# Performance work log

Hardware: AMD Instinct MI355X
Metric: run time of the kernel (lower is better)

Reference implementation:

```python
import jax, jax.numpy as jnp
import numpy as np

IN_DIM = 128
OUT_DIM = 256
N_ETYPES = 4
N_STEPS = 8
B = 128
N_NODES = 256
E = 393216
CONCAT = IN_DIM + OUT_DIM


def _conv1d(x, w, b):
    # x: [B, C, L], w: [O, I, K] -> valid conv, stride 1
    y = jax.lax.conv_general_dilated(x, w, (1,), 'VALID', dimension_numbers=('NCH', 'OIH', 'NCH'))
    return y + b[None, :, None]


def _maxpool1d(x, k, s):
    return jax.lax.reduce_window(x, -jnp.inf, jax.lax.max, (1, 1, k), (1, 1, s), 'VALID')


def setup_inputs():
    key = jax.random.key(0)
    ks = jax.random.split(key, 16)
    Nn = B * N_NODES
    sc = 0.05
    f32 = jnp.float32
    return {
        'features': jax.random.normal(ks[0], (Nn, IN_DIM), f32),
        'src': jax.random.randint(ks[1], (E,), 0, Nn),
        'dst': jax.random.randint(ks[2], (E,), 0, Nn),
        'etype': jax.random.randint(ks[3], (E,), 0, N_ETYPES),
        'W_msg': jax.random.normal(ks[4], (N_ETYPES, OUT_DIM, OUT_DIM), f32) * sc,
        'b_msg': jnp.zeros((N_ETYPES, OUT_DIM), f32),
        'gru_Wi': jax.random.normal(ks[5], (OUT_DIM, 3 * OUT_DIM), f32) * sc,
        'gru_Wh': jax.random.normal(ks[6], (OUT_DIM, 3 * OUT_DIM), f32) * sc,
        'gru_bi': jnp.zeros((3 * OUT_DIM,), f32),
        'gru_bh': jnp.zeros((3 * OUT_DIM,), f32),
        'conv1_w': jax.random.normal(ks[7], (OUT_DIM, OUT_DIM, 3), f32) * sc,
        'conv1_b': jnp.zeros((OUT_DIM,), f32),
        'conv2_w': jax.random.normal(ks[8], (OUT_DIM, OUT_DIM, 1), f32) * sc,
        'conv2_b': jnp.zeros((OUT_DIM,), f32),
        'convc1_w': jax.random.normal(ks[9], (CONCAT, CONCAT, 3), f32) * sc,
        'convc1_b': jnp.zeros((CONCAT,), f32),
        'convc2_w': jax.random.normal(ks[10], (CONCAT, CONCAT, 1), f32) * sc,
        'convc2_b': jnp.zeros((CONCAT,), f32),
        'wy': jax.random.normal(ks[11], (OUT_DIM, 1), f32) * sc,
        'by': jnp.zeros((1,), f32),
        'wz': jax.random.normal(ks[12], (CONCAT, 1), f32) * sc,
        'bz': jnp.zeros((1,), f32),
        'num_graphs': B,
    }


def reference(features, src, dst, etype, W_msg, b_msg, gru_Wi, gru_Wh, gru_bi, gru_bh,
              conv1_w, conv1_b, conv2_w, conv2_b, convc1_w, convc1_b, convc2_w, convc2_b,
              wy, by, wz, bz, num_graphs):
    Nn = features.shape[0]
    # DGL GatedGraphConv: pad input feats up to out_feats
    h = jnp.pad(features, ((0, 0), (0, OUT_DIM - IN_DIM)))
    for _ in range(N_STEPS):
        # per-etype linear transform of all nodes: [Nn, T, O]
        H_all = jnp.einsum('nd,tdo->nto', h, W_msg) + b_msg[None]
        msg = H_all[src, etype]                              # [E, O]
        a = jax.ops.segment_sum(msg, dst, num_segments=Nn)   # [Nn, O]
        gi = a @ gru_Wi + gru_bi
        gh = h @ gru_Wh + gru_bh
        ir, iz, ig = jnp.split(gi, 3, axis=-1)
        hr, hz, hg = jnp.split(gh, 3, axis=-1)
        r = jax.nn.sigmoid(ir + hr)
        z = jax.nn.sigmoid(iz + hz)
        g = jnp.tanh(ig + r * hg)
        h = (1.0 - z) * g + z * h
    x_i = features.reshape(num_graphs, -1, IN_DIM)
    h_i = h.reshape(num_graphs, -1, OUT_DIM)
    c_i = jnp.concatenate([h_i, x_i], axis=-1)
    Y1 = _maxpool1d(jax.nn.relu(_conv1d(h_i.transpose(0, 2, 1), conv1_w, conv1_b)), 3, 2)
    Y2 = _maxpool1d(jax.nn.relu(_conv1d(Y1, conv2_w, conv2_b)), 2, 2).transpose(0, 2, 1)
    Z1 = _maxpool1d(jax.nn.relu(_conv1d(c_i.transpose(0, 2, 1), convc1_w, convc1_b)), 3, 2)
    Z2 = _maxpool1d(jax.nn.relu(_conv1d(Z1, convc2_w, convc2_b)), 2, 2).transpose(0, 2, 1)
    before_avg = (Y2 @ wy + by) * (Z2 @ wz + bz)   # [B, L, 1]
    avg = before_avg.mean(axis=1)                    # [B, 1]
    return jax.nn.sigmoid(avg).squeeze(-1)           # [B]
```

## Files before the change

### kernel.cpp

```cpp
#include <hip/hip_runtime.h>

#define DEV static __device__ __forceinline__

typedef float f32x4 __attribute__((ext_vector_type(4)));
typedef __bf16 bf16x8 __attribute__((ext_vector_type(8)));
typedef unsigned int u32x4 __attribute__((ext_vector_type(4)));
typedef unsigned int u32x2 __attribute__((ext_vector_type(2)));

#define NNODE 32768
#define NEDGE 393216
#define EPAD (NEDGE + 8 * NNODE)

DEV unsigned short f2bf(float f) {
    unsigned int u = __builtin_bit_cast(unsigned int, f);
    u += 0x7FFFu + ((u >> 16) & 1u);
    return (unsigned short)(u >> 16);
}
DEV float bf2f(unsigned int b) {
    unsigned int u = b << 16;
    return __builtin_bit_cast(float, u);
}
DEV unsigned int pk2(float a, float b) {
    return (unsigned int)f2bf(a) | ((unsigned int)f2bf(b) << 16);
}
DEV float sigf(float x) { return 1.f / (1.f + __expf(-x)); }

DEV void gld16(const void* g, void* l) {
    __builtin_amdgcn_global_load_lds(
        (const __attribute__((address_space(1))) void*)(g),
        (__attribute__((address_space(3))) void*)(l),
        16, 0, 0);
}


__global__ __launch_bounds__(256) void init_k(
    const float* __restrict__ feat,
    unsigned short* __restrict__ hb0, unsigned short* __restrict__ hb1,
    unsigned short* __restrict__ fb)
{
    int idx = blockIdx.x * 256 + threadIdx.x;
    int r = idx >> 8, c = idx & 255;
    float f = 0.f;
    if (r < NNODE && c < 128) f = feat[(size_t)r * 128 + c];
    unsigned short v = f2bf(f);
    hb0[(size_t)r * 256 + c] = v;
    hb1[(size_t)r * 256 + c] = v;
    if (c < 128) fb[(size_t)r * 128 + c] = v;
}

__global__ __launch_bounds__(256) void prep_wmsg_k(
    const float* __restrict__ Wm, unsigned short* __restrict__ WT)
{
    int idx = blockIdx.x * 256 + threadIdx.x;
    int j = idx >> 8, d = idx & 255;
    int t = j >> 8, o = j & 255;
    WT[idx] = f2bf(Wm[t * 65536 + d * 256 + o]);
}

__global__ __launch_bounds__(256) void prep_gru_k(
    const float* __restrict__ Wi, const float* __restrict__ Wh,
    unsigned short* __restrict__ B2T)
{
    int idx = blockIdx.x * 256 + threadIdx.x;
    int j = idx >> 9, k = idx & 511;
    int band = j >> 6, g = (j >> 4) & 3, ch = (band << 4) + (j & 15);
    float v = 0.f;
    if (g == 0) v = (k < 256) ? Wi[k * 768 + ch] : Wh[(k - 256) * 768 + ch];
    else if (g == 1) v = (k < 256) ? Wi[k * 768 + 256 + ch] : Wh[(k - 256) * 768 + 256 + ch];
    else if (g == 2) { if (k < 256) v = Wi[k * 768 + 512 + ch]; }
    else { if (k >= 256) v = Wh[(k - 256) * 768 + 512 + ch]; }
    B2T[idx] = f2bf(v);
}

__global__ __launch_bounds__(256) void prep_bias2_k(
    const float* __restrict__ bi, const float* __restrict__ bh,
    float* __restrict__ b2)
{
    int j = blockIdx.x * 256 + threadIdx.x;
    int band = j >> 6, g = (j >> 4) & 3, ch = (band << 4) + (j & 15);
    float v;
    if (g == 0) v = bi[ch] + bh[ch];
    else if (g == 1) v = bi[256 + ch] + bh[256 + ch];
    else if (g == 2) v = bi[512 + ch];
    else v = bh[512 + ch];
    b2[j] = v;
}

__global__ __launch_bounds__(256) void prep_conv_k(
    const float* __restrict__ c1w, const float* __restrict__ c2w,
    const float* __restrict__ cc1w, const float* __restrict__ cc2w,
    unsigned short* __restrict__ BTY, unsigned short* __restrict__ BT2,
    unsigned short* __restrict__ BTZ, unsigned short* __restrict__ BTc2)
{
    int idx = blockIdx.x * 256 + threadIdx.x;
    if (idx < 196608) {
        int o = idx / 768, kk = idx - o * 768, k = kk >> 8, c = kk & 255;
        BTY[idx] = f2bf(c1w[o * 768 + c * 3 + k]);
    } else if (idx < 262144) {
        int r = idx - 196608, o = r >> 8, c = r & 255;
        BT2[r] = f2bf(c2w[o * 256 + c]);
    } else if (idx < 704512) {
        int jx = idx - 262144, o = jx / 1152, kk = jx - o * 1152;
        float v;
        if (kk < 768) { int k = kk >> 8, c = kk & 255; v = cc1w[o * 1152 + c * 3 + k]; }
        else { int r = kk - 768, kf = r >> 7, cf = r & 127; v = cc1w[o * 1152 + (256 + cf) * 3 + kf]; }
        BTZ[jx] = f2bf(v);
    } else {
        int r = idx - 704512, o = r / 384, c = r - o * 384;
        BTc2[r] = f2bf(cc2w[o * 384 + c]);
    }
}


__global__ __launch_bounds__(256) void pad_k(int* __restrict__ edat)
{
    edat[blockIdx.x * 256 + threadIdx.x] = NNODE;
}

__global__ __launch_bounds__(256) void count_k(
    const int* __restrict__ dst, int* __restrict__ cnt)
{
    int e = blockIdx.x * 256 + threadIdx.x;
    atomicAdd(&cnt[dst[e]], 1);
}

__global__ __launch_bounds__(1024) void scan1_k(
    const int* __restrict__ cnt, int* __restrict__ rp, int* __restrict__ bsum)
{
    __shared__ int buf[1024];
    int b = blockIdx.x, tid = threadIdx.x;
    int n = (b << 10) + tid;
    int v = (cnt[n] + 7) & ~7;
    buf[tid] = v;
    __syncthreads();
    for (int off = 1; off < 1024; off <<= 1) {
        int x = (tid >= off) ? buf[tid - off] : 0;
        __syncthreads();
        buf[tid] += x;
        __syncthreads();
    }
    rp[n] = buf[tid] - v;
    if (tid == 1023) bsum[b] = buf[1023];
}

__global__ __launch_bounds__(64) void scan2_k(
    const int* __restrict__ bsum, int* __restrict__ boff, int* __restrict__ rp)
{
    int lane = threadIdx.x;
    int v = (lane < 32) ? bsum[lane] : 0;
    int s = v;
    #pragma unroll
    for (int off = 1; off < 32; off <<= 1) {
        int x = __shfl_up(s, off, 64);
        if (lane >= off) s += x;
    }
    if (lane < 32) boff[lane] = s - v;
    if (lane == 31) rp[NNODE] = s;
}

__global__ __launch_bounds__(1024) void scan3_k(
    int* __restrict__ rp, const int* __restrict__ boff)
{
    int b = blockIdx.x, tid = threadIdx.x;
    rp[(b << 10) + tid] += boff[b];
}

__global__ __launch_bounds__(256) void fill_k(
    const int* __restrict__ src, const int* __restrict__ dst,
    const int* __restrict__ et, const int* __restrict__ rp,
    int* __restrict__ pos, int* __restrict__ edat)
{
    int e = blockIdx.x * 256 + threadIdx.x;
    int d = dst[e];
    int p = atomicAdd(&pos[d], 1);
    edat[rp[d] + p] = src[e] | (et[e] << 20);
}


__global__ __launch_bounds__(256) void agg2_k(
    const int* __restrict__ rp, const int* __restrict__ edat,
    const unsigned short* __restrict__ Hmsg, unsigned short* __restrict__ Aonly)
{
    int wave = threadIdx.x >> 6, lane = threadIdx.x & 63;
    int n = (blockIdx.x << 2) + wave;
    int e0 = rp[n], e1 = rp[n + 1];
    float a0 = 0.f, a1 = 0.f, a2 = 0.f, a3 = 0.f;
    const unsigned short* hc = Hmsg + (lane << 2);
    for (int e = e0; e < e1; e += 8) {
        u32x2 v[8];
        #pragma unroll
        for (int q = 0; q < 8; q++) {
            int d = edat[e + q];
            v[q] = *(const u32x2*)(hc + ((size_t)(d & 0xFFFFF) << 10) + ((d >> 20) << 8));
        }
        #pragma unroll
        for (int q = 0; q < 8; q++) {
            a0 += bf2f(v[q].x & 0xFFFFu); a1 += bf2f(v[q].x >> 16);
            a2 += bf2f(v[q].y & 0xFFFFu); a3 += bf2f(v[q].y >> 16);
        }
    }
    u32x2 p; p.x = pk2(a0, a1); p.y = pk2(a2, a3);
    *(u32x2*)(Aonly + (size_t)n * 256 + (lane << 2)) = p;
}

#define STAGE_COORDS                                            \
    int srow[4], scb[4], soff[4];                               \
    _Pragma("unroll")                                           \
    for (int p = 0; p < 4; p++) {                               \
        int c = wave + p * 4;                                   \
        int half = c >> 3, cc = c & 7;                          \
        srow[p] = cc * 16 + (lane >> 2);                        \
        scb[p] = (((lane & 3) ^ ((lane >> 3) & 3)) + half * 4) * 8; \
        soff[p] = half * 4096 + cc * 512;                       \
    }

#define MFMA64(AS, BS)                                                        \
    _Pragma("unroll")                                                         \
    for (int h = 0; h < 2; h++) {                                             \
        bf16x8 af[4], bfr[4];                                                 \
        _Pragma("unroll")                                                     \
        for (int i = 0; i < 4; i++)                                           \
            af[i] = *(const bf16x8*)(&(AS)[h * 4096 + (qm + i * 16 + fm) * 32 + fksw * 8]); \
        _Pragma("unroll")                                                     \
        for (int i = 0; i < 4; i++)                                           \
            bfr[i] = *(const bf16x8*)(&(BS)[h * 4096 + (qn + i * 16 + fm) * 32 + fksw * 8]); \
        _Pragma("unroll")                                                     \
        for (int i = 0; i < 4; i++)                                           \
            _Pragma("unroll")                                                 \
            for (int j = 0; j < 4; j++)                                       \
                acc[i][j] = __builtin_amdgcn_mfma_f32_16x16x32_bf16(bfr[j], af[i], acc[i][j], 0, 0, 0); \
    }

#define MFMA64G(AS, BS, SK)                                                   \
    _Pragma("unroll")                                                         \
    for (int h = 0; h < 2; h++) {                                             \
        bf16x8 af[4], bfr[4];                                                 \
        _Pragma("unroll")                                                     \
        for (int i = 0; i < 4; i++)                                           \
            af[i] = *(const bf16x8*)(&(AS)[h * 4096 + (qm + i * 16 + fm) * 32 + fksw * 8]); \
        _Pragma("unroll")                                                     \
        for (int j = 0; j < 4; j++) {                                         \
            if (j == (SK)) continue;                                          \
            bfr[j] = *(const bf16x8*)(&(BS)[h * 4096 + (qn + j * 16 + fm) * 32 + fksw * 8]); \
        }                                                                     \
        _Pragma("unroll")                                                     \
        for (int i = 0; i < 4; i++)                                           \
            _Pragma("unroll")                                                 \
            for (int j = 0; j < 4; j++) {                                     \
                if (j == (SK)) continue;                                      \
                acc[i][j] = __builtin_amdgcn_mfma_f32_16x16x32_bf16(bfr[j], af[i], acc[i][j], 0, 0, 0); \
            }                                                                 \
    }

__global__ __launch_bounds__(256) void gemm_hmsg(
    const unsigned short* __restrict__ A,
    const unsigned short* __restrict__ Bt,
    unsigned short* __restrict__ Cb,
    const float* __restrict__ bias)
{
    __shared__ __align__(16) unsigned short As0[128 * 64];
    __shared__ __align__(16) unsigned short As1[128 * 64];
    __shared__ __align__(16) unsigned short Bs0[128 * 64];
    __shared__ __align__(16) unsigned short Bs1[128 * 64];
    const int tid = threadIdx.x;
    int id = blockIdx.x;
    { int per = gridDim.x >> 3; id = (id & 7) * per + (id >> 3); }
    const int bm = id >> 3, bn = id & 7;
    const int wave = tid >> 6, lane = tid & 63;
    const unsigned short* Ag = A + (size_t)(bm * 128) * 256;
    const unsigned short* Bg = Bt + (size_t)(bn * 128) * 256;
    const int qm = (wave & 1) << 6, qn = (wave >> 1) << 6;
    const int fm = lane & 15, fkv = lane >> 4;
    const int fksw = fkv ^ ((fm >> 1) & 3);
    STAGE_COORDS

    auto stageA = [&](int kb, unsigned short* dst) {
        #pragma unroll
        for (int p = 0; p < 4; p++)
            gld16(Ag + (size_t)srow[p] * 256 + kb + scb[p], dst + soff[p]);
    };
    auto stageB = [&](int kb, unsigned short* dst) {
        #pragma unroll
        for (int p = 0; p < 4; p++)
            gld16(Bg + (size_t)srow[p] * 256 + kb + scb[p], dst + soff[p]);
    };

    f32x4 acc[4][4] = {};

    stageA(0, As0); stageB(0, Bs0);
    __syncthreads();
    unsigned short *Ac = As0, *An = As1, *Bc = Bs0, *Bn = Bs1;
    #pragma unroll
    for (int kb = 0; kb < 256; kb += 64) {
        if (kb < 192) { stageA(kb + 64, An); stageB(kb + 64, Bn); }
        MFMA64(Ac, Bc)
        __syncthreads();
        { auto t = Ac; Ac = An; An = t; }
        { auto t = Bc; Bc = Bn; Bn = t; }
    }

    const int m0 = bm * 128 + qm + fm;
    const int n0 = bn * 128 + qn + (fkv << 2);
    #pragma unroll
    for (int i = 0; i < 4; i++) {
        int row = m0 + i * 16;
        #pragma unroll
        for (int j = 0; j < 4; j++) {
            int col = n0 + j * 16;
            float4 bv = *(const float4*)(bias + col);
            u32x2 p;
            p.x = pk2(acc[i][j][0] + bv.x, acc[i][j][1] + bv.y);
            p.y = pk2(acc[i][j][2] + bv.z, acc[i][j][3] + bv.w);
            *(u32x2*)(Cb + (size_t)row * 1024 + col) = p;
        }
    }
}

__global__ __launch_bounds__(256) void gemm_bt(
    const unsigned short* __restrict__ A, int lda,
    const unsigned short* __restrict__ Bt,
    unsigned short* __restrict__ Cb, int ldcb,
    const float* __restrict__ bias,
    int N, int K, int swz, int relu)
{
    __shared__ __align__(16) unsigned short As0[128 * 64];
    __shared__ __align__(16) unsigned short As1[128 * 64];
    __shared__ __align__(16) unsigned short Bs0[128 * 64];
    __shared__ __align__(16) unsigned short Bs1[128 * 64];
    const int tid = threadIdx.x;
    int id = blockIdx.x;
    if (swz) { int per = gridDim.x >> 3; id = (id & 7) * per + (id >> 3); }
    const int nb = N >> 7;
    const int bm = id / nb, bn = id - bm * nb;
    const int wave = tid >> 6, lane = tid & 63;
    const unsigned short* Ag = A + (size_t)(bm * 128) * lda;
    const unsigned short* Bg = Bt + (size_t)(bn * 128) * K;
    const int qm = (wave & 1) << 6, qn = (wave >> 1) << 6;
    const int fm = lane & 15, fkv = lane >> 4;
    const int fksw = fkv ^ ((fm >> 1) & 3);
    STAGE_COORDS

    auto stageA = [&](int kb, unsigned short* dst) {
        #pragma unroll
        for (int p = 0; p < 4; p++)
            gld16(Ag + (size_t)srow[p] * lda + kb + scb[p], dst + soff[p]);
    };
    auto stageB = [&](int kb, unsigned short* dst) {
        #pragma unroll
        for (int p = 0; p < 4; p++)
            gld16(Bg + (size_t)srow[p] * K + kb + scb[p], dst + soff[p]);
    };

    f32x4 acc[4][4] = {};

    stageA(0, As0); stageB(0, Bs0);
    __syncthreads();
    unsigned short *Ac = As0, *An = As1, *Bc = Bs0, *Bn = Bs1;
    for (int kb = 0; kb < K; kb += 64) {
        if (kb + 64 < K) { stageA(kb + 64, An); stageB(kb + 64, Bn); }
        MFMA64(Ac, Bc)
        __syncthreads();
        { auto t = Ac; Ac = An; An = t; }
        { auto t = Bc; Bc = Bn; Bn = t; }
    }

    const int m0 = bm * 128 + qm + fm;
    const int n0 = bn * 128 + qn + (fkv << 2);
    #pragma unroll
    for (int i = 0; i < 4; i++) {
        int row = m0 + i * 16;
        #pragma unroll
        for (int j = 0; j < 4; j++) {
            int col = n0 + j * 16;
            float v0 = acc[i][j][0], v1 = acc[i][j][1],
                  v2 = acc[i][j][2], v3 = acc[i][j][3];
            if (bias) {
                float4 bv = *(const float4*)(bias + col);
                v0 += bv.x; v1 += bv.y; v2 += bv.z; v3 += bv.w;
            }
            if (relu) {
                v0 = fmaxf(v0, 0.f); v1 = fmaxf(v1, 0.f);
                v2 = fmaxf(v2, 0.f); v3 = fmaxf(v3, 0.f);
            }
            u32x2 p; p.x = pk2(v0, v1); p.y = pk2(v2, v3);
            *(u32x2*)(Cb + (size_t)row * ldcb + col) = p;
        }
    }
}

__global__ __launch_bounds__(256) void gemm_conv(
    const unsigned short* __restrict__ Ah,
    const unsigned short* __restrict__ Af,
    const unsigned short* __restrict__ Bt,
    unsigned short* __restrict__ Cb, int ldcb,
    const float* __restrict__ bias,
    int N, int K)
{
    __shared__ __align__(16) unsigned short As0[128 * 64];
    __shared__ __align__(16) unsigned short As1[128 * 64];
    __shared__ __align__(16) unsigned short Bs0[128 * 64];
    __shared__ __align__(16) unsigned short Bs1[128 * 64];
    const int tid = threadIdx.x;
    int id = blockIdx.x;
    { int per = gridDim.x >> 3; id = (id & 7) * per + (id >> 3); }
    const int nb = N >> 7;
    const int bm = id / nb, bn = id - bm * nb;
    const int wave = tid >> 6, lane = tid & 63;
    const unsigned short* Bg = Bt + (size_t)(bn * 128) * K;
    const int qm = (wave & 1) << 6, qn = (wave >> 1) << 6;
    const int fm = lane & 15, fkv = lane >> 4;
    const int fksw = fkv ^ ((fm >> 1) & 3);
    STAGE_COORDS

    auto stageA = [&](int kb, unsigned short* dst) {
        const unsigned short* base; int ldA, col, shift;
        if (kb < 768) { base = Ah; ldA = 256; shift = kb >> 8; col = kb & 255; }
        else { int r = kb - 768; base = Af; ldA = 128; shift = r >> 7; col = r & 127; }
        const unsigned short* Ag = base + (size_t)(bm * 128 + shift) * ldA + col;
        #pragma unroll
        for (int p = 0; p < 4; p++)
            gld16(Ag + (size_t)srow[p] * ldA + scb[p], dst + soff[p]);
    };
    auto stageB = [&](int kb, unsigned short* dst) {
        #pragma unroll
        for (int p = 0; p < 4; p++)
            gld16(Bg + (size_t)srow[p] * K + kb + scb[p], dst + soff[p]);
    };

    f32x4 acc[4][4] = {};

    stageA(0, As0); stageB(0, Bs0);
    __syncthreads();
    unsigned short *Ac = As0, *An = As1, *Bc = Bs0, *Bn = Bs1;
    for (int kb = 0; kb < K; kb += 64) {
        if (kb + 64 < K) { stageA(kb + 64, An); stageB(kb + 64, Bn); }
        MFMA64(Ac, Bc)
        __syncthreads();
        { auto t = Ac; Ac = An; An = t; }
        { auto t = Bc; Bc = Bn; Bn = t; }
    }

    const int m0 = bm * 128 + qm + fm;
    const int n0 = bn * 128 + qn + (fkv << 2);
    #pragma unroll
    for (int i = 0; i < 4; i++) {
        int row = m0 + i * 16;
        #pragma unroll
        for (int j = 0; j < 4; j++) {
            int col = n0 + j * 16;
            float4 bv = *(const float4*)(bias + col);
            float v0 = fmaxf(acc[i][j][0] + bv.x, 0.f);
            float v1 = fmaxf(acc[i][j][1] + bv.y, 0.f);
            float v2 = fmaxf(acc[i][j][2] + bv.z, 0.f);
            float v3 = fmaxf(acc[i][j][3] + bv.w, 0.f);
            u32x2 p; p.x = pk2(v0, v1); p.y = pk2(v2, v3);
            *(u32x2*)(Cb + (size_t)row * ldcb + col) = p;
        }
    }
}

__global__ __launch_bounds__(256) void gemm_gru(
    const unsigned short* __restrict__ Aonly,
    const unsigned short* __restrict__ hbc,
    const unsigned short* __restrict__ Bt,
    const float* __restrict__ b2p,
    unsigned short* __restrict__ hbn)
{
    __shared__ __align__(16) unsigned short As0[128 * 64];
    __shared__ __align__(16) unsigned short As1[128 * 64];
    __shared__ __align__(16) unsigned short Bs0[128 * 64];
    __shared__ __align__(16) unsigned short Bs1[128 * 64];
    const int tid = threadIdx.x;
    int id = blockIdx.x;
    { int per = gridDim.x >> 3; id = (id & 7) * per + (id >> 3); }
    const int bm = id >> 3;
    const int bn = id & 7;
    const int wave = tid >> 6, lane = tid & 63;
    const unsigned short* Bg = Bt + (size_t)(bn * 128) * 512;
    const int qm = (wave & 1) << 6, qn = (wave >> 1) << 6;
    const int fm = lane & 15, fkv = lane >> 4;
    const int fksw = fkv ^ ((fm >> 1) & 3);
    STAGE_COORDS

    auto stageA = [&](int kb, unsigned short* dst) {
        const unsigned short* base = (kb < 256) ? Aonly : hbc;
        const unsigned short* Ag = base + (size_t)(bm * 128) * 256 + (kb & 255);
        #pragma unroll
        for (int p = 0; p < 4; p++)
            gld16(Ag + (size_t)srow[p] * 256 + scb[p], dst + soff[p]);
    };
    auto stageB = [&](int kb, unsigned short* dst) {
        #pragma unroll
        for (int p = 0; p < 4; p++)
            gld16(Bg + (size_t)srow[p] * 512 + kb + scb[p], dst + soff[p]);
    };

    f32x4 acc[4][4] = {};

    stageA(0, As0); stageB(0, Bs0);
    __syncthreads();
    unsigned short *Ac = As0, *An = As1, *Bc = Bs0, *Bn = Bs1;
    #pragma unroll
    for (int kb = 0; kb < 512; kb += 64) {
        if (kb < 448) { stageA(kb + 64, An); stageB(kb + 64, Bn); }
        if (kb < 256) { MFMA64G(Ac, Bc, 3) }
        else          { MFMA64G(Ac, Bc, 2) }
        __syncthreads();
        { auto t = Ac; Ac = An; An = t; }
        { auto t = Bc; Bc = Bn; Bn = t; }
    }

    const int band = (bn << 1) + (qn >> 6);
    const int chb = (band << 4) + (fkv << 2);
    const float4 brv = *(const float4*)(b2p + (band << 6) + 0  + (fkv << 2));
    const float4 bzv = *(const float4*)(b2p + (band << 6) + 16 + (fkv << 2));
    const float4 bgv = *(const float4*)(b2p + (band << 6) + 32 + (fkv << 2));
    const float4 bhv = *(const float4*)(b2p + (band << 6) + 48 + (fkv << 2));
    const float br_[4] = {brv.x, brv.y, brv.z, brv.w};
    const float bz_[4] = {bzv.x, bzv.y, bzv.z, bzv.w};
    const float bg_[4] = {bgv.x, bgv.y, bgv.z, bgv.w};
    const float bh_[4] = {bhv.x, bhv.y, bhv.z, bhv.w};
    const int m0 = bm * 128 + qm + fm;
    #pragma unroll
    for (int i = 0; i < 4; i++) {
        int row = m0 + i * 16;
        u32x2 hv = *(const u32x2*)(hbc + (size_t)row * 256 + chb);
        float hp[4] = {bf2f(hv.x & 0xFFFFu), bf2f(hv.x >> 16),
                       bf2f(hv.y & 0xFFFFu), bf2f(hv.y >> 16)};
        float hn[4];
        #pragma unroll
        for (int r = 0; r < 4; r++) {
            float rg = sigf(acc[i][0][r] + br_[r]);
            float zz = sigf(acc[i][1][r] + bz_[r]);
            float pre = acc[i][2][r] + bg_[r] + rg * (acc[i][3][r] + bh_[r]);
            pre = fminf(fmaxf(pre, -15.f), 15.f);
            float t = __expf(2.f * pre);
            float gq = (t - 1.f) / (t + 1.f);
            hn[r] = (1.f - zz) * gq + zz * hp[r];
        }
        u32x2 p; p.x = pk2(hn[0], hn[1]); p.y = pk2(hn[2], hn[3]);
        *(u32x2*)(hbn + (size_t)row * 256 + chb) = p;
    }
}

__global__ __launch_bounds__(256) void pool_k(
    const unsigned short* __restrict__ in, int ldin, int Lb_in, int L_out,
    int win, int C,
    unsigned short* __restrict__ ob, int ldo)
{
    int idx = blockIdx.x * 256 + threadIdx.x;
    int c = idx % C;
    int row = idx / C;
    int b = row / L_out, lp = row - b * L_out;
    const unsigned short* p = in + (size_t)(b * Lb_in + 2 * lp) * ldin + c;
    float m = bf2f(p[0]);
    for (int d = 1; d < win; d++) m = fmaxf(m, bf2f(p[(size_t)d * ldin]));
    ob[(size_t)row * ldo + c] = f2bf(m);
}

__global__ __launch_bounds__(64) void final_k(
    const unsigned short* __restrict__ CY, const unsigned short* __restrict__ CZ,
    const float* __restrict__ wy, const float* __restrict__ by,
    const float* __restrict__ wz, const float* __restrict__ bz,
    float* __restrict__ out)
{
    int b = blockIdx.x, lane = threadIdx.x;
    float val = 0.f;
    if (lane < 63) {
        const unsigned short* y0 = CY + (size_t)(b * 126 + 2 * lane) * 256;
        const unsigned short* y1 = y0 + 256;
        float y = 0.f;
        for (int o = 0; o < 256; o++)
            y += fmaxf(bf2f(y0[o]), bf2f(y1[o])) * wy[o];
        y += by[0];
        const unsigned short* z0 = CZ + (size_t)(b * 126 + 2 * lane) * 384;
        const unsigned short* z1 = z0 + 384;
        float z = 0.f;
        for (int o = 0; o < 384; o++)
            z += fmaxf(bf2f(z0[o]), bf2f(z1[o])) * wz[o];
        z += bz[0];
        val = y * z;
    }
    for (int off = 32; off > 0; off >>= 1) val += __shfl_down(val, off, 64);
    if (lane == 0) out[b] = sigf(val * (1.f / 63.f));
}


extern "C" void kernel_launch(void* const* d_in, const int* in_sizes, int n_in,
                              void* d_out, int out_size, void* d_ws, size_t ws_size,
                              hipStream_t stream)
{
    const float* feat = (const float*)d_in[0];
    const int* src = (const int*)d_in[1];
    const int* dst = (const int*)d_in[2];
    const int* et  = (const int*)d_in[3];
    const float* Wm  = (const float*)d_in[4];
    const float* bm  = (const float*)d_in[5];
    const float* Wi  = (const float*)d_in[6];
    const float* Wh  = (const float*)d_in[7];
    const float* bi  = (const float*)d_in[8];
    const float* bh  = (const float*)d_in[9];
    const float* c1w = (const float*)d_in[10];
    const float* c1b = (const float*)d_in[11];
    const float* c2w = (const float*)d_in[12];
    const float* c2b = (const float*)d_in[13];
    const float* cc1w = (const float*)d_in[14];
    const float* cc1b = (const float*)d_in[15];
    const float* cc2w = (const float*)d_in[16];
    const float* cc2b = (const float*)d_in[17];
    const float* wy = (const float*)d_in[18];
    const float* by = (const float*)d_in[19];
    const float* wz = (const float*)d_in[20];
    const float* bz = (const float*)d_in[21];
    float* out = (float*)d_out;

    char* w = (char*)d_ws;
    size_t off = 0;
    auto alloc = [&](size_t bytes) -> char* {
        char* p = w + off; off += (bytes + 255) & ~(size_t)255; return p;
    };
    unsigned short* hb0 = (unsigned short*)alloc((size_t)(NNODE + 8) * 256 * 2);
    unsigned short* hb1 = (unsigned short*)alloc((size_t)(NNODE + 8) * 256 * 2);
    unsigned short* fb  = (unsigned short*)alloc((size_t)(NNODE + 8) * 128 * 2);
    unsigned short* Aonly = (unsigned short*)alloc((size_t)NNODE * 256 * 2);
    char* R = alloc((size_t)(NNODE + 1) * 1024 * 2);
    unsigned short* Hmsg = (unsigned short*)R;
    unsigned short* CbY  = (unsigned short*)R;
    unsigned short* CbZ  = (unsigned short*)(R + (size_t)NNODE * 256 * 2);
    unsigned short* P    = (unsigned short*)alloc((size_t)16128 * 384 * 2);
    unsigned short* Cb2Y = (unsigned short*)alloc((size_t)16128 * 256 * 2);
    unsigned short* Cb2Z = (unsigned short*)alloc((size_t)16128 * 384 * 2);
    unsigned short* WT   = (unsigned short*)alloc(1024 * 256 * 2);
    unsigned short* B2T  = (unsigned short*)alloc(1024 * 512 * 2);
    float* b2            = (float*)alloc(1024 * 4);
    unsigned short* BTY  = (unsigned short*)alloc(256 * 768 * 2);
    unsigned short* BT2  = (unsigned short*)alloc(256 * 256 * 2);
    unsigned short* BTZ  = (unsigned short*)alloc(384 * 1152 * 2);
    unsigned short* BTc2 = (unsigned short*)alloc(384 * 384 * 2);
    int* rp     = (int*)alloc((NNODE + 1) * 4);
    int* pos    = (int*)alloc(NNODE * 4);
    int* cnt    = (int*)alloc(NNODE * 4);
    int* bsum   = (int*)alloc(32 * 4);
    int* boff   = (int*)alloc(32 * 4);
    int* edat   = (int*)alloc((size_t)EPAD * 4);

    hipLaunchKernelGGL(init_k, dim3(NNODE + 8), dim3(256), 0, stream, feat, hb0, hb1, fb);
    hipLaunchKernelGGL(prep_wmsg_k, dim3(1024), dim3(256), 0, stream, Wm, WT);
    hipLaunchKernelGGL(prep_gru_k, dim3(2048), dim3(256), 0, stream, Wi, Wh, B2T);
    hipLaunchKernelGGL(prep_bias2_k, dim3(4), dim3(256), 0, stream, bi, bh, b2);
    hipLaunchKernelGGL(prep_conv_k, dim3(3328), dim3(256), 0, stream,
                       c1w, c2w, cc1w, cc2w, BTY, BT2, BTZ, BTc2);
    hipMemsetAsync(pos, 0, NNODE * 4, stream);
    hipMemsetAsync(cnt, 0, NNODE * 4, stream);
    hipMemsetAsync(Hmsg + (size_t)NNODE * 1024, 0, 1024 * 2, stream);
    hipLaunchKernelGGL(pad_k, dim3(EPAD / 256), dim3(256), 0, stream, edat);
    hipLaunchKernelGGL(count_k, dim3(NEDGE / 256), dim3(256), 0, stream, dst, cnt);
    hipLaunchKernelGGL(scan1_k, dim3(32), dim3(1024), 0, stream, cnt, rp, bsum);
    hipLaunchKernelGGL(scan2_k, dim3(1), dim3(64), 0, stream, bsum, boff, rp);
    hipLaunchKernelGGL(scan3_k, dim3(32), dim3(1024), 0, stream, rp, boff);
    hipLaunchKernelGGL(fill_k, dim3(NEDGE / 256), dim3(256), 0, stream, src, dst, et, rp, pos, edat);

    unsigned short* hbuf[2] = {hb0, hb1};
    for (int step = 0; step < 8; step++) {
        unsigned short* cur = hbuf[step & 1];
        unsigned short* nxt = hbuf[(step + 1) & 1];
        hipLaunchKernelGGL(gemm_hmsg, dim3(2048), dim3(256), 0, stream,
            cur, WT, Hmsg, bm);
        hipLaunchKernelGGL(agg2_k, dim3(NNODE / 4), dim3(256), 0, stream, rp, edat, Hmsg, Aonly);
        hipLaunchKernelGGL(gemm_gru, dim3(2048), dim3(256), 0, stream,
            Aonly, cur, B2T, b2, nxt);
    }

    hipLaunchKernelGGL(gemm_conv, dim3(512), dim3(256), 0, stream,
        hb0, (const unsigned short*)nullptr, BTY, CbY, 256, c1b, 256, 768);
    hipLaunchKernelGGL(pool_k, dim3(16128), dim3(256), 0, stream,
        CbY, 256, 256, 126, 3, 256, P, 256);
    hipLaunchKernelGGL(gemm_bt, dim3(252), dim3(256), 0, stream,
        P, 256, BT2, Cb2Y, 256, c2b, 256, 256, 0, 1);

    hipLaunchKernelGGL(gemm_conv, dim3(768), dim3(256), 0, stream,
        hb0, fb, BTZ, CbZ, 384, cc1b, 384, 1152);
    hipLaunchKernelGGL(pool_k, dim3(24192), dim3(256), 0, stream,
        CbZ, 384, 256, 126, 3, 384, P, 384);
    hipLaunchKernelGGL(gemm_bt, dim3(378), dim3(256), 0, stream,
        P, 384, BTc2, Cb2Z, 384, cc2b, 384, 384, 0, 1);

    hipLaunchKernelGGL(final_k, dim3(128), dim3(64), 0, stream,
        Cb2Y, Cb2Z, wy, by, wz, bz, out);
}
```

Measured before the change: 1.192 ms.

## Fuse prep kernels, widen aggregation loads, skip zero-padded K in first step

Merges the four weight-prep kernels into one launch and folds the edge-padding fill into the count kernel. The block-offset scan pass is removed; consumers add the block offset themselves. Aggregation now uses 16-byte loads with two edges per lane-half, padding segments to 16 and combining halves with a shuffle. Step 0 GEMMs skip the zero upper half of the padded input K-range, and the final reduction is parallelised across 256 threads. Padding to 16 adds dummy edge reads for low-degree nodes.

```diff
diff --git a/kernel.cpp b/kernel.cpp
--- a/kernel.cpp
+++ b/kernel.cpp
@@ -9,7 +9,7 @@
 
 #define NNODE 32768
 #define NEDGE 393216
-#define EPAD (NEDGE + 8 * NNODE)
+#define EPAD (NEDGE + 16 * NNODE)
 
 DEV unsigned short f2bf(float f) {
     unsigned int u = __builtin_bit_cast(unsigned int, f);
@@ -48,80 +48,70 @@
     if (c < 128) fb[(size_t)r * 128 + c] = v;
 }
 
-__global__ __launch_bounds__(256) void prep_wmsg_k(
-    const float* __restrict__ Wm, unsigned short* __restrict__ WT)
-{
-    int idx = blockIdx.x * 256 + threadIdx.x;
-    int j = idx >> 8, d = idx & 255;
-    int t = j >> 8, o = j & 255;
-    WT[idx] = f2bf(Wm[t * 65536 + d * 256 + o]);
-}
-
-__global__ __launch_bounds__(256) void prep_gru_k(
+__global__ __launch_bounds__(256) void prep_all_k(
+    const float* __restrict__ Wm,
     const float* __restrict__ Wi, const float* __restrict__ Wh,
-    unsigned short* __restrict__ B2T)
-{
-    int idx = blockIdx.x * 256 + threadIdx.x;
-    int j = idx >> 9, k = idx & 511;
-    int band = j >> 6, g = (j >> 4) & 3, ch = (band << 4) + (j & 15);
-    float v = 0.f;
-    if (g == 0) v = (k < 256) ? Wi[k * 768 + ch] : Wh[(k - 256) * 768 + ch];
-    else if (g == 1) v = (k < 256) ? Wi[k * 768 + 256 + ch] : Wh[(k - 256) * 768 + 256 + ch];
-    else if (g == 2) { if (k < 256) v = Wi[k * 768 + 512 + ch]; }
-    else { if (k >= 256) v = Wh[(k - 256) * 768 + 512 + ch]; }
-    B2T[idx] = f2bf(v);
-}
-
-__global__ __launch_bounds__(256) void prep_bias2_k(
     const float* __restrict__ bi, const float* __restrict__ bh,
-    float* __restrict__ b2)
-{
-    int j = blockIdx.x * 256 + threadIdx.x;
-    int band = j >> 6, g = (j >> 4) & 3, ch = (band << 4) + (j & 15);
-    float v;
-    if (g == 0) v = bi[ch] + bh[ch];
-    else if (g == 1) v = bi[256 + ch] + bh[256 + ch];
-    else if (g == 2) v = bi[512 + ch];
-    else v = bh[512 + ch];
-    b2[j] = v;
-}
-
-__global__ __launch_bounds__(256) void prep_conv_k(
     const float* __restrict__ c1w, const float* __restrict__ c2w,
     const float* __restrict__ cc1w, const float* __restrict__ cc2w,
+    unsigned short* __restrict__ WT, unsigned short* __restrict__ B2T,
+    float* __restrict__ b2,
     unsigned short* __restrict__ BTY, unsigned short* __restrict__ BT2,
     unsigned short* __restrict__ BTZ, unsigned short* __restrict__ BTc2)
 {
-    int idx = blockIdx.x * 256 + threadIdx.x;
-    if (idx < 196608) {
-        int o = idx / 768, kk = idx - o * 768, k = kk >> 8, c = kk & 255;
-        BTY[idx] = f2bf(c1w[o * 768 + c * 3 + k]);
-    } else if (idx < 262144) {
-        int r = idx - 196608, o = r >> 8, c = r & 255;
-        BT2[r] = f2bf(c2w[o * 256 + c]);
-    } else if (idx < 704512) {
-        int jx = idx - 262144, o = jx / 1152, kk = jx - o * 1152;
+    int gid = blockIdx.x * 256 + threadIdx.x;
+    if (gid < 262144) {
+        int idx = gid;
+        int j = idx >> 8, d = idx & 255;
+        int t = j >> 8, o = j & 255;
+        WT[idx] = f2bf(Wm[t * 65536 + d * 256 + o]);
+    } else if (gid < 786432) {
+        int idx = gid - 262144;
+        int j = idx >> 9, k = idx & 511;
+        int band = j >> 6, g = (j >> 4) & 3, ch = (band << 4) + (j & 15);
+        float v = 0.f;
+        if (g == 0) v = (k < 256) ? Wi[k * 768 + ch] : Wh[(k - 256) * 768 + ch];
+        else if (g == 1) v = (k < 256) ? Wi[k * 768 + 256 + ch] : Wh[(k - 256) * 768 + 256 + ch];
+        else if (g == 2) { if (k < 256) v = Wi[k * 768 + 512 + ch]; }
+        else { if (k >= 256) v = Wh[(k - 256) * 768 + 512 + ch]; }
+        B2T[idx] = f2bf(v);
+    } else if (gid < 787456) {
+        int j = gid - 786432;
+        int band = j >> 6, g = (j >> 4) & 3, ch = (band << 4) + (j & 15);
         float v;
-        if (kk < 768) { int k = kk >> 8, c = kk & 255; v = cc1w[o * 1152 + c * 3 + k]; }
-        else { int r = kk - 768, kf = r >> 7, cf = r & 127; v = cc1w[o * 1152 + (256 + cf) * 3 + kf]; }
-        BTZ[jx] = f2bf(v);
+        if (g == 0) v = bi[ch] + bh[ch];
+        else if (g == 1) v = bi[256 + ch] + bh[256 + ch];
+        else if (g == 2) v = bi[512 + ch];
+        else v = bh[512 + ch];
+        b2[j] = v;
     } else {
-        int r = idx - 704512, o = r / 384, c = r - o * 384;
-        BTc2[r] = f2bf(cc2w[o * 384 + c]);
-    }
-}
-
-
-__global__ __launch_bounds__(256) void pad_k(int* __restrict__ edat)
-{
-    edat[blockIdx.x * 256 + threadIdx.x] = NNODE;
-}
-
-__global__ __launch_bounds__(256) void count_k(
-    const int* __restrict__ dst, int* __restrict__ cnt)
+        int idx = gid - 787456;
+        if (idx < 196608) {
+            int o = idx / 768, kk = idx - o * 768, k = kk >> 8, c = kk & 255;
+            BTY[idx] = f2bf(c1w[o * 768 + c * 3 + k]);
+        } else if (idx < 262144) {
+            int r = idx - 196608, o = r >> 8, c = r & 255;
+            BT2[r] = f2bf(c2w[o * 256 + c]);
+        } else if (idx < 704512) {
+            int jx = idx - 262144, o = jx / 1152, kk = jx - o * 1152;
+            float v;
+            if (kk < 768) { int k = kk >> 8, c = kk & 255; v = cc1w[o * 1152 + c * 3 + k]; }
+            else { int r = kk - 768, kf = r >> 7, cf = r & 127; v = cc1w[o * 1152 + (256 + cf) * 3 + kf]; }
+            BTZ[jx] = f2bf(v);
+        } else {
+            int r = idx - 704512, o = r / 384, c = r - o * 384;
+            BTc2[r] = f2bf(cc2w[o * 384 + c]);
+        }
+    }
+}
+
+
+__global__ __launch_bounds__(256) void pc_k(
+    const int* __restrict__ dst, int* __restrict__ cnt, int* __restrict__ edat)
 {
     int e = blockIdx.x * 256 + threadIdx.x;
-    atomicAdd(&cnt[dst[e]], 1);
+    edat[e] = NNODE;
+    if (e < NEDGE) atomicAdd(&cnt[dst[e]], 1);
 }
 
 __global__ __launch_bounds__(1024) void scan1_k(
@@ -130,7 +120,7 @@
     __shared__ int buf[1024];
     int b = blockIdx.x, tid = threadIdx.x;
     int n = (b << 10) + tid;
-    int v = (cnt[n] + 7) & ~7;
+    int v = (cnt[n] + 15) & ~15;
     buf[tid] = v;
     __syncthreads();
     for (int off = 1; off < 1024; off <<= 1) {
@@ -155,52 +145,61 @@
         if (lane >= off) s += x;
     }
     if (lane < 32) boff[lane] = s - v;
+    if (lane == 32) boff[32] = 0;
     if (lane == 31) rp[NNODE] = s;
-}
-
-__global__ __launch_bounds__(1024) void scan3_k(
-    int* __restrict__ rp, const int* __restrict__ boff)
-{
-    int b = blockIdx.x, tid = threadIdx.x;
-    rp[(b << 10) + tid] += boff[b];
 }
 
 __global__ __launch_bounds__(256) void fill_k(
     const int* __restrict__ src, const int* __restrict__ dst,
     const int* __restrict__ et, const int* __restrict__ rp,
+    const int* __restrict__ boff,
     int* __restrict__ pos, int* __restrict__ edat)
 {
     int e = blockIdx.x * 256 + threadIdx.x;
     int d = dst[e];
     int p = atomicAdd(&pos[d], 1);
-    edat[rp[d] + p] = src[e] | (et[e] << 20);
+    edat[rp[d] + boff[d >> 10] + p] = src[e] | (et[e] << 20);
 }
 
 
 __global__ __launch_bounds__(256) void agg2_k(
-    const int* __restrict__ rp, const int* __restrict__ edat,
+    const int* __restrict__ rp, const int* __restrict__ boff,
+    const int* __restrict__ edat,
     const unsigned short* __restrict__ Hmsg, unsigned short* __restrict__ Aonly)
 {
     int wave = threadIdx.x >> 6, lane = threadIdx.x & 63;
     int n = (blockIdx.x << 2) + wave;
-    int e0 = rp[n], e1 = rp[n + 1];
+    int e0 = rp[n] + boff[n >> 10];
+    int e1 = rp[n + 1] + boff[(n + 1) >> 10];
+    int half = lane >> 5, lc = lane & 31;
     float a0 = 0.f, a1 = 0.f, a2 = 0.f, a3 = 0.f;
-    const unsigned short* hc = Hmsg + (lane << 2);
-    for (int e = e0; e < e1; e += 8) {
-        u32x2 v[8];
+    float a4 = 0.f, a5 = 0.f, a6 = 0.f, a7 = 0.f;
+    const unsigned short* hc = Hmsg + (lc << 3);
+    for (int e = e0; e < e1; e += 16) {
+        u32x4 v[8];
         #pragma unroll
         for (int q = 0; q < 8; q++) {
-            int d = edat[e + q];
-            v[q] = *(const u32x2*)(hc + ((size_t)(d & 0xFFFFF) << 10) + ((d >> 20) << 8));
+            int d = edat[e + (q << 1) + half];
+            v[q] = *(const u32x4*)(hc + ((size_t)(d & 0xFFFFF) << 10) + ((d >> 20) << 8));
         }
         #pragma unroll
         for (int q = 0; q < 8; q++) {
             a0 += bf2f(v[q].x & 0xFFFFu); a1 += bf2f(v[q].x >> 16);
             a2 += bf2f(v[q].y & 0xFFFFu); a3 += bf2f(v[q].y >> 16);
+            a4 += bf2f(v[q].z & 0xFFFFu); a5 += bf2f(v[q].z >> 16);
+            a6 += bf2f(v[q].w & 0xFFFFu); a7 += bf2f(v[q].w >> 16);
         }
     }
-    u32x2 p; p.x = pk2(a0, a1); p.y = pk2(a2, a3);
-    *(u32x2*)(Aonly + (size_t)n * 256 + (lane << 2)) = p;
+    a0 += __shfl_xor(a0, 32, 64); a1 += __shfl_xor(a1, 32, 64);
+    a2 += __shfl_xor(a2, 32, 64); a3 += __shfl_xor(a3, 32, 64);
+    a4 += __shfl_xor(a4, 32, 64); a5 += __shfl_xor(a5, 32, 64);
+    a6 += __shfl_xor(a6, 32, 64); a7 += __shfl_xor(a7, 32, 64);
+    if (half == 0) {
+        u32x4 p;
+        p.x = pk2(a0, a1); p.y = pk2(a2, a3);
+        p.z = pk2(a4, a5); p.w = pk2(a6, a7);
+        *(u32x4*)(Aonly + (size_t)n * 256 + (lc << 3)) = p;
+    }
 }
 
 #define STAGE_COORDS                                            \
@@ -252,6 +251,7 @@
             }                                                                 \
     }
 
+template<int NT>
 __global__ __launch_bounds__(256) void gemm_hmsg(
     const unsigned short* __restrict__ A,
     const unsigned short* __restrict__ Bt,
@@ -291,8 +291,8 @@
     __syncthreads();
     unsigned short *Ac = As0, *An = As1, *Bc = Bs0, *Bn = Bs1;
     #pragma unroll
-    for (int kb = 0; kb < 256; kb += 64) {
-        if (kb < 192) { stageA(kb + 64, An); stageB(kb + 64, Bn); }
+    for (int kb = 0; kb < NT * 64; kb += 64) {
+        if (kb + 64 < NT * 64) { stageA(kb + 64, An); stageB(kb + 64, Bn); }
         MFMA64(Ac, Bc)
         __syncthreads();
         { auto t = Ac; Ac = An; An = t; }
@@ -459,6 +459,7 @@
     }
 }
 
+template<int NT>
 __global__ __launch_bounds__(256) void gemm_gru(
     const unsigned short* __restrict__ Aonly,
     const unsigned short* __restrict__ hbc,
@@ -501,8 +502,8 @@
     __syncthreads();
     unsigned short *Ac = As0, *An = As1, *Bc = Bs0, *Bn = Bs1;
     #pragma unroll
-    for (int kb = 0; kb < 512; kb += 64) {
-        if (kb < 448) { stageA(kb + 64, An); stageB(kb + 64, Bn); }
+    for (int kb = 0; kb < NT * 64; kb += 64) {
+        if (kb + 64 < NT * 64) { stageA(kb + 64, An); stageB(kb + 64, Bn); }
         if (kb < 256) { MFMA64G(Ac, Bc, 3) }
         else          { MFMA64G(Ac, Bc, 2) }
         __syncthreads();
@@ -558,31 +559,48 @@
     ob[(size_t)row * ldo + c] = f2bf(m);
 }
 
-__global__ __launch_bounds__(64) void final_k(
+__global__ __launch_bounds__(256) void final_k(
     const unsigned short* __restrict__ CY, const unsigned short* __restrict__ CZ,
     const float* __restrict__ wy, const float* __restrict__ by,
     const float* __restrict__ wz, const float* __restrict__ bz,
     float* __restrict__ out)
 {
-    int b = blockIdx.x, lane = threadIdx.x;
-    float val = 0.f;
-    if (lane < 63) {
-        const unsigned short* y0 = CY + (size_t)(b * 126 + 2 * lane) * 256;
+    __shared__ float ws[4];
+    int b = blockIdx.x, tid = threadIdx.x;
+    int wave = tid >> 6, lane = tid & 63;
+    float wyv[4], wzv[6];
+    #pragma unroll
+    for (int j = 0; j < 4; j++) wyv[j] = wy[lane * 4 + j];
+    #pragma unroll
+    for (int j = 0; j < 6; j++) wzv[j] = wz[lane * 6 + j];
+    const float byv = by[0], bzv = bz[0];
+    float acc = 0.f;
+    for (int l = wave; l < 63; l += 4) {
+        const unsigned short* y0 = CY + (size_t)(b * 126 + 2 * l) * 256 + lane * 4;
         const unsigned short* y1 = y0 + 256;
-        float y = 0.f;
-        for (int o = 0; o < 256; o++)
-            y += fmaxf(bf2f(y0[o]), bf2f(y1[o])) * wy[o];
-        y += by[0];
-        const unsigned short* z0 = CZ + (size_t)(b * 126 + 2 * lane) * 384;
+        u32x2 u0 = *(const u32x2*)y0, u1 = *(const u32x2*)y1;
+        float py =
+            fmaxf(bf2f(u0.x & 0xFFFFu), bf2f(u1.x & 0xFFFFu)) * wyv[0] +
+            fmaxf(bf2f(u0.x >> 16),     bf2f(u1.x >> 16))     * wyv[1] +
+            fmaxf(bf2f(u0.y & 0xFFFFu), bf2f(u1.y & 0xFFFFu)) * wyv[2] +
+            fmaxf(bf2f(u0.y >> 16),     bf2f(u1.y >> 16))     * wyv[3];
+        const unsigned short* z0 = CZ + (size_t)(b * 126 + 2 * l) * 384 + lane * 6;
         const unsigned short* z1 = z0 + 384;
-        float z = 0.f;
-        for (int o = 0; o < 384; o++)
-            z += fmaxf(bf2f(z0[o]), bf2f(z1[o])) * wz[o];
-        z += bz[0];
-        val = y * z;
-    }
-    for (int off = 32; off > 0; off >>= 1) val += __shfl_down(val, off, 64);
-    if (lane == 0) out[b] = sigf(val * (1.f / 63.f));
+        float pz = 0.f;
+        #pragma unroll
+        for (int j = 0; j < 6; j++)
+            pz += fmaxf(bf2f(z0[j]), bf2f(z1[j])) * wzv[j];
+        #pragma unroll
+        for (int off = 32; off > 0; off >>= 1) {
+            py += __shfl_down(py, off, 64);
+            pz += __shfl_down(pz, off, 64);
+        }
+        if (lane == 0) acc += (py + byv) * (pz + bzv);
+    }
+    if (lane == 0) ws[wave] = acc;
+    __syncthreads();
+    if (tid == 0)
+        out[b] = sigf((ws[0] + ws[1] + ws[2] + ws[3]) * (1.f / 63.f));
 }
 
 
@@ -641,34 +659,40 @@
     int* pos    = (int*)alloc(NNODE * 4);
     int* cnt    = (int*)alloc(NNODE * 4);
     int* bsum   = (int*)alloc(32 * 4);
-    int* boff   = (int*)alloc(32 * 4);
+    int* boff   = (int*)alloc(33 * 4);
     int* edat   = (int*)alloc((size_t)EPAD * 4);
 
     hipLaunchKernelGGL(init_k, dim3(NNODE + 8), dim3(256), 0, stream, feat, hb0, hb1, fb);
-    hipLaunchKernelGGL(prep_wmsg_k, dim3(1024), dim3(256), 0, stream, Wm, WT);
-    hipLaunchKernelGGL(prep_gru_k, dim3(2048), dim3(256), 0, stream, Wi, Wh, B2T);
-    hipLaunchKernelGGL(prep_bias2_k, dim3(4), dim3(256), 0, stream, bi, bh, b2);
-    hipLaunchKernelGGL(prep_conv_k, dim3(3328), dim3(256), 0, stream,
-                       c1w, c2w, cc1w, cc2w, BTY, BT2, BTZ, BTc2);
+    hipLaunchKernelGGL(prep_all_k, dim3(6404), dim3(256), 0, stream,
+                       Wm, Wi, Wh, bi, bh, c1w, c2w, cc1w, cc2w,
+                       WT, B2T, b2, BTY, BT2, BTZ, BTc2);
     hipMemsetAsync(pos, 0, NNODE * 4, stream);
     hipMemsetAsync(cnt, 0, NNODE * 4, stream);
     hipMemsetAsync(Hmsg + (size_t)NNODE * 1024, 0, 1024 * 2, stream);
-    hipLaunchKernelGGL(pad_k, dim3(EPAD / 256), dim3(256), 0, stream, edat);
-    hipLaunchKernelGGL(count_k, dim3(NEDGE / 256), dim3(256), 0, stream, dst, cnt);
+    hipLaunchKernelGGL(pc_k, dim3(EPAD / 256), dim3(256), 0, stream, dst, cnt, edat);
     hipLaunchKernelGGL(scan1_k, dim3(32), dim3(1024), 0, stream, cnt, rp, bsum);
     hipLaunchKernelGGL(scan2_k, dim3(1), dim3(64), 0, stream, bsum, boff, rp);
-    hipLaunchKernelGGL(scan3_k, dim3(32), dim3(1024), 0, stream, rp, boff);
-    hipLaunchKernelGGL(fill_k, dim3(NEDGE / 256), dim3(256), 0, stream, src, dst, et, rp, pos, edat);
+    hipLaunchKernelGGL(fill_k, dim3(NEDGE / 256), dim3(256), 0, stream,
+                       src, dst, et, rp, boff, pos, edat);
 
     unsigned short* hbuf[2] = {hb0, hb1};
     for (int step = 0; step < 8; step++) {
         unsigned short* cur = hbuf[step & 1];
         unsigned short* nxt = hbuf[(step + 1) & 1];
-        hipLaunchKernelGGL(gemm_hmsg, dim3(2048), dim3(256), 0, stream,
-            cur, WT, Hmsg, bm);
-        hipLaunchKernelGGL(agg2_k, dim3(NNODE / 4), dim3(256), 0, stream, rp, edat, Hmsg, Aonly);
-        hipLaunchKernelGGL(gemm_gru, dim3(2048), dim3(256), 0, stream,
-            Aonly, cur, B2T, b2, nxt);
+        if (step == 0)
+            hipLaunchKernelGGL((gemm_hmsg<2>), dim3(2048), dim3(256), 0, stream,
+                cur, WT, Hmsg, bm);
+        else
+            hipLaunchKernelGGL((gemm_hmsg<4>), dim3(2048), dim3(256), 0, stream,
+                cur, WT, Hmsg, bm);
+        hipLaunchKernelGGL(agg2_k, dim3(NNODE / 4), dim3(256), 0, stream,
+            rp, boff, edat, Hmsg, Aonly);
+        if (step == 0)
+            hipLaunchKernelGGL((gemm_gru<6>), dim3(2048), dim3(256), 0, stream,
+                Aonly, cur, B2T, b2, nxt);
+        else
+            hipLaunchKernelGGL((gemm_gru<8>), dim3(2048), dim3(256), 0, stream,
+                Aonly, cur, B2T, b2, nxt);
     }
 
     hipLaunchKernelGGL(gemm_conv, dim3(512), dim3(256), 0, stream,
@@ -685,6 +709,6 @@
     hipLaunchKernelGGL(gemm_bt, dim3(378), dim3(256), 0, stream,
         P, 384, BTc2, Cb2Z, 384, cc2b, 384, 384, 0, 1);
 
-    hipLaunchKernelGGL(final_k, dim3(128), dim3(64), 0, stream,
+    hipLaunchKernelGGL(final_k, dim3(128), dim3(256), 0, stream,
         Cb2Y, Cb2Z, wy, by, wz, bz, out);
 }
```

New measurement: 1.139 ms. -4.5%, faster.
